# Performance work log

Measured on AMD Instinct MI355X. Metric: run time of the kernel, lower is better.

Reference implementation:

```python
import jax, jax.numpy as jnp
import numpy as np

B, N, OBS, H, HEADS = 8192, 32, 128, 256, 4
HD = H // HEADS  # head dim = 64
GAIN = (0.125 / H) ** 0.5
LN_EPS = 1e-5


def _ln(x):
    # LayerNorm over last dim, no affine (elementwise_affine=False)
    m = x.mean(axis=-1, keepdims=True)
    v = ((x - m) ** 2).mean(axis=-1, keepdims=True)
    return (x - m) * jax.lax.rsqrt(v + LN_EPS)


def setup_inputs() -> dict:
    key = jax.random.key(0)
    ks = jax.random.split(key, 20)
    f32 = jnp.float32
    # weights stored (in, out) so y = x @ W + b (transpose of torch layout)
    def w(k, i, o, g):
        return (jax.random.normal(k, (i, o), dtype=f32) * g)
    inp = {
        "all_agent_obs": jax.random.normal(ks[0], (B, N, OBS), dtype=f32),
        # EntityEmbedding (obs-only): 1-layer LinearEncoder, normal init * t-fixup gain
        "W_emb": w(ks[1], OBS, H, GAIN), "b_emb": jnp.zeros((H,), f32),
        # ResidualSelfAttention projections
        "Wq": w(ks[2], H, H, GAIN), "bq": jnp.zeros((H,), f32),
        "Wk": w(ks[3], H, H, GAIN), "bk": jnp.zeros((H,), f32),
        "Wv": w(ks[4], H, H, GAIN), "bv": jnp.zeros((H,), f32),
        "Wo": w(ks[5], H, H, GAIN), "bo": jnp.zeros((H,), f32),
        # LinearEncoder tail (num_layers=2), kaiming-ish scale * t-fixup gain
        "W1": w(ks[6], H, H, GAIN), "b1": jnp.zeros((H,), f32),
        "W2": w(ks[7], H, H, GAIN), "b2": jnp.zeros((H,), f32),
        # value head: Linear(h_size + 1, 1)
        "Wval": w(ks[8], H + 1, 1, (1.0 / (H + 1)) ** 0.5), "bval": jnp.zeros((1,), f32),
    }
    return inp


def reference(all_agent_obs, W_emb, b_emb, Wq, bq, Wk, bk, Wv, bv, Wo, bo,
              W1, b1, W2, b2, Wval, bval):
    # --- EntityEmbedding: 1-layer MLP with SiLU ---
    ent = jax.nn.silu(jnp.einsum("bno,oh->bnh", all_agent_obs, W_emb) + b_emb)

    # --- ResidualSelfAttention (pre-norm, no mask) ---
    x = _ln(ent)                                        # embedding_norm
    q = (x @ Wq + bq).reshape(B, N, HEADS, HD)
    k = (x @ Wk + bk).reshape(B, N, HEADS, HD)
    v = (x @ Wv + bv).reshape(B, N, HEADS, HD)
    attn = jnp.einsum("bnhd,bmhd->bhnm", q, k) / jnp.sqrt(jnp.float32(HD))
    attn = jax.nn.softmax(attn, axis=-1)
    out = jnp.einsum("bhnm,bmhd->bnhd", attn, v).reshape(B, N, H)
    out = _ln(out @ Wo + bo + x)                        # fc_out + residual, residual_norm
    pooled = out.mean(axis=1)                           # (B, H) unmasked avg pool

    # --- LinearEncoder tail (2 layers, SiLU) ---
    enc = jax.nn.silu(pooled @ W1 + b1)
    enc = jax.nn.silu(enc @ W2 + b2)

    # --- norm agent count: max_agents updates to N, so val = N*2/N - 1 = 1.0 ---
    nc = jnp.ones((B, 1), dtype=enc.dtype)
    enc = jnp.concatenate([enc, nc], axis=-1)           # (B, H+1)
    return enc @ Wval + bval                            # (B, 1)
```

## Files before the change

kernel.cpp:

```cpp
#include <hip/hip_runtime.h>


typedef __bf16 bf16x8 __attribute__((ext_vector_type(8)));
typedef float f32x4 __attribute__((ext_vector_type(4)));
typedef unsigned short ushort_t;

#define DEVI static __device__ __forceinline__
#define MFMA16(a, b, cc) __builtin_amdgcn_mfma_f32_16x16x32_bf16((a), (b), (cc), 0, 0, 0)

#define WAITV2 asm volatile("s_waitcnt vmcnt(2)" ::: "memory")
#define WAITV0 asm volatile("s_waitcnt vmcnt(0)" ::: "memory")
#define WAITLG asm volatile("s_waitcnt lgkmcnt(0)" ::: "memory")
#define BAR() __builtin_amdgcn_s_barrier()
#define SCHEDB() __builtin_amdgcn_sched_barrier(0)

constexpr int OWemb_ = 0;
constexpr int OWq_   = 32768;
constexpr int OWk_   = OWq_ + 65536;
constexpr int OWv_   = OWk_ + 65536;
constexpr int OWo_   = OWv_ + 65536;
constexpr int OW1_   = OWo_ + 65536;
constexpr int OW2_   = OW1_ + 65536;

constexpr int OBS_STRIDE = 264;
constexpr int L_BST = 32768;
constexpr int LDS_TOTAL = 32768 + 3 * 16384;
static_assert(LDS_TOTAL <= 81920, "need <=80KB for 2 blocks/CU");

DEVI float silu_f(float x) { return x / (1.0f + __expf(-x)); }
DEVI f32x4 splat4(float x) { f32x4 v = {x, x, x, x}; return v; }
DEVI uint2 pack4(f32x4 v) {
  union { __bf16 h[4]; uint2 u; } x;
  x.h[0] = (__bf16)v[0]; x.h[1] = (__bf16)v[1];
  x.h[2] = (__bf16)v[2]; x.h[3] = (__bf16)v[3];
  return x.u;
}
DEVI f32x4 unpk(uint2 u) {
  union { uint2 u2; __bf16 h[4]; } x; x.u2 = u;
  f32x4 v = {(float)x.h[0], (float)x.h[1], (float)x.h[2], (float)x.h[3]};
  return v;
}
DEVI bf16x8 ld_frag(const char* p) { return *(const bf16x8*)p; }
DEVI bf16x8 u4b(unsigned a, unsigned b, unsigned cc, unsigned d) {
  union { unsigned u[4]; bf16x8 v; } x;
  x.u[0] = a; x.u[1] = b; x.u[2] = cc; x.u[3] = d;
  return x.v;
}
DEVI unsigned to_agpr(unsigned v) {
  unsigned d;
  asm volatile("v_accvgpr_write_b32 %0, %1" : "=a"(d) : "v"(v));
  return d;
}
DEVI unsigned from_agpr(unsigned a) {
  unsigned d;
  asm volatile("v_accvgpr_read_b32 %0, %1" : "=v"(d) : "a"(a));
  return d;
}
DEVI int xaddr(int row, int k4) {
  int t = row >> 4, cc = row & 15;
  int ks = k4 >> 5, kg = (k4 >> 3) & 3, half = (k4 >> 2) & 1;
  return ((t * 8 + ks) * 64 + kg * 16 + cc) * 16 + half * 8;
}

typedef const __attribute__((address_space(1))) unsigned int* gas_ptr;
typedef __attribute__((address_space(3))) unsigned int* las_ptr;
DEVI void gload16(const void* g, void* l) {
  __builtin_amdgcn_global_load_lds((gas_ptr)g, (las_ptr)l, 16, 0, 0);
}

constexpr int CSRC(int p) {
  return (p < 4)  ? (OWemb_ + p * 8192)
       : (p < 12) ? (OWq_ + (p - 4) * 8192)
       : (p < 20) ? (OWk_ + (p - 12) * 8192)
       : (p < 28) ? (OWv_ + (p - 20) * 8192)
                  : (OWo_ + (p - 28) * 8192);
}

DEVI void issue_chunk(const ushort_t* pw, int srcOff, char* bst, int slot, int wv, int lane) {
  char* dst = bst + slot * 16384 + wv * 2048;
  const ushort_t* s = pw + srcOff + wv * 1024 + (size_t)lane * 8;
  gload16(s, dst);
  gload16(s + 512, dst + 1024);
}
#define PH_ISSUE(ch) issue_chunk(pw, CSRC(ch), bst, (ch) % 3, wv, lane)

__global__ void pack_weights(const float* __restrict__ Wemb, const float* __restrict__ Wq,
                             const float* __restrict__ Wk, const float* __restrict__ Wv,
                             const float* __restrict__ Wo, const float* __restrict__ W1,
                             const float* __restrict__ W2, ushort_t* __restrict__ ws) {
  int t = blockIdx.x * 256 + threadIdx.x;
  if (t >= 53248) return;
  const float* src;
  int dst, n, k0;
  if (t < 4096) {
    int rem = t & 1023;
    int ctg = rem >> 6, l = rem & 63;
    n = ctg * 16 + (l & 15);
    k0 = (t >> 10) * 32 + (l >> 4) * 8;
    src = Wemb; dst = OWemb_ + t * 8;
  } else if (t < 36864) {
    int u = t - 4096, m = u >> 13, loc = u & 8191;
    int rem = loc & 1023;
    int ctg = rem >> 6, l = rem & 63;
    n = ctg * 16 + (l & 15);
    k0 = (loc >> 10) * 32 + (l >> 4) * 8;
    src = (m == 0) ? Wq : (m == 1) ? Wk : (m == 2) ? Wv : Wo;
    dst = OWq_ + m * 65536 + loc * 8;
  } else {
    int u = t - 36864, m = u >> 13, loc = u & 8191;
    int ln = loc & 63, ks = (loc >> 6) & 7, ct = loc >> 9;
    n = ct * 16 + (ln & 15);
    k0 = ks * 32 + (ln >> 4) * 8;
    src = m ? W2 : W1; dst = OW1_ + m * 65536 + loc * 8;
  }
  union { __bf16 h[8]; uint4 u; } pk;
  #pragma unroll
  for (int j = 0; j < 8; ++j) pk.h[j] = (__bf16)src[(k0 + j) * 256 + n];
  *(uint4*)(ws + dst) = pk.u;
}

__global__ __launch_bounds__(512, 4)
void poca_fused(const float* __restrict__ obs, const ushort_t* __restrict__ pw,
                const float* __restrict__ b_emb, const float* __restrict__ bq,
                const float* __restrict__ bk, const float* __restrict__ bv,
                const float* __restrict__ bo, const float* __restrict__ b1,
                const float* __restrict__ b2, const float* __restrict__ Wval,
                const float* __restrict__ bval, float* __restrict__ out) {
  __shared__ __align__(128) char lds[LDS_TOTAL];
  const int tid = threadIdx.x;
  const int wv = tid >> 6, lane = tid & 63;
  const int g = lane >> 4, c = lane & 15;
  const int mg = wv >> 2, ng = wv & 3;
  char* xb = lds;
  char* bst = lds + L_BST;
  char* as_ = bst + wv * 4096;
  char* pp1 = bst;
  char* poolb = bst;
  char* y1b = bst + 8448;
  char* ptlb = bst + 16896;
  char* pp2 = bst + 20480;

  PH_ISSUE(0); PH_ISSUE(1);
  f32x4 bemb_r[4];
  #pragma unroll
  for (int ct = 0; ct < 4; ++ct) bemb_r[ct] = *(const f32x4*)(b_emb + ng * 64 + ct * 16 + g * 4);

  {
    const float4* op = (const float4*)(obs + (size_t)blockIdx.x * 64 * 128);
    #pragma unroll
    for (int it = 0; it < 4; ++it) {
      int idx = it * 512 + tid;
      float4 v = op[idx];
      int row = idx >> 5, col4 = idx & 31;
      union { __bf16 h[4]; uint2 u; } cv;
      cv.h[0] = (__bf16)v.x; cv.h[1] = (__bf16)v.y;
      cv.h[2] = (__bf16)v.z; cv.h[3] = (__bf16)v.w;
      *(uint2*)(xb + row * OBS_STRIDE + col4 * 8) = cv.u;
    }
  }
  WAITLG;

  f32x4 acc[2][4];

  #pragma unroll
  for (int p = 0; p < 4; ++p) {
    WAITV2; BAR();
    PH_ISSUE(p + 2);
    if (p == 0) {
      #pragma unroll
      for (int ct = 0; ct < 4; ++ct) { acc[0][ct] = bemb_r[ct]; acc[1][ct] = bemb_r[ct]; }
    }
    const char* ck = bst + (p % 3) * 16384;
    bf16x8 wf[4], xf[2];
    #pragma unroll
    for (int t = 0; t < 4; ++t) wf[t] = ld_frag(ck + ((ng * 4 + t) * 64 + lane) * 16);
    #pragma unroll
    for (int rt = 0; rt < 2; ++rt)
      xf[rt] = ld_frag(xb + ((mg * 2 + rt) * 16 + c) * OBS_STRIDE + p * 64 + g * 16);
    #pragma unroll
    for (int rt = 0; rt < 2; ++rt)
      #pragma unroll
      for (int ct = 0; ct < 4; ++ct) acc[rt][ct] = MFMA16(wf[ct], xf[rt], acc[rt][ct]);
    SCHEDB();
  }

  BAR();
  #pragma unroll
  for (int rt = 0; rt < 2; ++rt)
    #pragma unroll
    for (int ct = 0; ct < 4; ++ct)
      #pragma unroll
      for (int r = 0; r < 4; ++r) acc[rt][ct][r] = silu_f(acc[rt][ct][r]);
  #pragma unroll
  for (int rt = 0; rt < 2; ++rt) {
    float s1 = 0.f, s2 = 0.f;
    #pragma unroll
    for (int ct = 0; ct < 4; ++ct)
      #pragma unroll
      for (int r = 0; r < 4; ++r) { float e = acc[rt][ct][r]; s1 += e; s2 += e * e; }
    s1 += __shfl_xor(s1, 16); s2 += __shfl_xor(s2, 16);
    s1 += __shfl_xor(s1, 32); s2 += __shfl_xor(s2, 32);
    if (g == 0)
      *(float2*)(pp1 + (mg * 32 + rt * 16 + c) * 32 + ng * 8) = make_float2(s1, s2);
  }
  WAITLG; BAR();
  {
    float mu[2], rs[2];
    #pragma unroll
    for (int rt = 0; rt < 2; ++rt) {
      int row = mg * 32 + rt * 16 + c;
      f32x4 pA = *(const f32x4*)(pp1 + row * 32);
      f32x4 pB = *(const f32x4*)(pp1 + row * 32 + 16);
      float S1 = pA[0] + pA[2] + pB[0] + pB[2];
      float S2 = pA[1] + pA[3] + pB[1] + pB[3];
      float m_ = S1 * (1.f / 256.f);
      float v_ = S2 * (1.f / 256.f) - m_ * m_;
      mu[rt] = m_; rs[rt] = rsqrtf(v_ + 1e-5f);
    }
    #pragma unroll
    for (int rt = 0; rt < 2; ++rt)
      #pragma unroll
      for (int ct = 0; ct < 4; ++ct) {
        f32x4 xv;
        #pragma unroll
        for (int r = 0; r < 4; ++r) xv[r] = (acc[rt][ct][r] - mu[rt]) * rs[rt];
        *(uint2*)(xb + xaddr(mg * 32 + rt * 16 + c, ng * 64 + ct * 16 + g * 4)) = pack4(xv);
      }
  }
  f32x4 bq_r[4];
  #pragma unroll
  for (int ct = 0; ct < 4; ++ct) bq_r[ct] = *(const f32x4*)(bq + ng * 64 + ct * 16 + g * 4);
  SCHEDB();
  WAITLG; BAR();

  #pragma unroll
  for (int p = 4; p < 12; ++p) {
    WAITV2; BAR();
    PH_ISSUE(p + 2);
    if (p == 4) {
      #pragma unroll
      for (int ct = 0; ct < 4; ++ct) { acc[0][ct] = bq_r[ct]; acc[1][ct] = bq_r[ct]; }
    }
    const char* ck = bst + (p % 3) * 16384;
    const int ks = p - 4;
    bf16x8 wf[4], xf[2];
    #pragma unroll
    for (int t = 0; t < 4; ++t) wf[t] = ld_frag(ck + ((ng * 4 + t) * 64 + lane) * 16);
    #pragma unroll
    for (int rt = 0; rt < 2; ++rt)
      xf[rt] = ld_frag(xb + (((mg * 2 + rt) * 8 + ks) * 64 + lane) * 16);
    #pragma unroll
    for (int rt = 0; rt < 2; ++rt)
      #pragma unroll
      for (int ct = 0; ct < 4; ++ct) acc[rt][ct] = MFMA16(wf[ct], xf[rt], acc[rt][ct]);
    SCHEDB();
  }

  unsigned qs[16];
  #pragma unroll
  for (int rt = 0; rt < 2; ++rt)
    #pragma unroll
    for (int ct = 0; ct < 4; ++ct) {
      uint2 qp = pack4(acc[rt][ct]);
      qs[(rt * 4 + ct) * 2] = to_agpr(qp.x);
      qs[(rt * 4 + ct) * 2 + 1] = to_agpr(qp.y);
    }
  f32x4 bk_r[4];
  #pragma unroll
  for (int ct = 0; ct < 4; ++ct) bk_r[ct] = *(const f32x4*)(bk + ng * 64 + ct * 16 + g * 4);

  #pragma unroll
  for (int p = 12; p < 20; ++p) {
    if (p < 19) { WAITV2; } else { WAITV0; }
    BAR();
    if (p <= 17) PH_ISSUE(p + 2);
    if (p == 12) {
      #pragma unroll
      for (int ct = 0; ct < 4; ++ct) { acc[0][ct] = bk_r[ct]; acc[1][ct] = bk_r[ct]; }
    }
    const char* ck = bst + (p % 3) * 16384;
    const int ks = p - 12;
    bf16x8 wf[4], xf[2];
    #pragma unroll
    for (int t = 0; t < 4; ++t) wf[t] = ld_frag(ck + ((ng * 4 + t) * 64 + lane) * 16);
    #pragma unroll
    for (int rt = 0; rt < 2; ++rt)
      xf[rt] = ld_frag(xb + (((mg * 2 + rt) * 8 + ks) * 64 + lane) * 16);
    #pragma unroll
    for (int rt = 0; rt < 2; ++rt)
      #pragma unroll
      for (int ct = 0; ct < 4; ++ct) acc[rt][ct] = MFMA16(wf[ct], xf[rt], acc[rt][ct]);
    SCHEDB();
  }

  float rinv[2];
  uint2 p_pk[2][2];
  float bv_r[4];
  {
    BAR();
    f32x4 sacc[2][2];
    sacc[0][0] = splat4(0.f); sacc[0][1] = splat4(0.f);
    sacc[1][0] = splat4(0.f); sacc[1][1] = splat4(0.f);
    #pragma unroll
    for (int hf = 0; hf < 2; ++hf) {
      #pragma unroll
      for (int rt2 = 0; rt2 < 2; ++rt2)
        #pragma unroll
        for (int ctl = 0; ctl < 2; ++ctl) {
          int gr = ctl * 2 + (g >> 1);
          int off = rt2 * 1024 + (gr * 16 + c) * 16 + (g & 1) * 8;
          int qi = (rt2 * 4 + hf * 2 + ctl) * 2;
          *(uint2*)(as_ + off) = make_uint2(from_agpr(qs[qi]), from_agpr(qs[qi + 1]));
          *(uint2*)(as_ + 2048 + off) = pack4(acc[rt2][hf * 2 + ctl]);
        }
      WAITLG;
      bf16x8 qf[2], kf[2];
      #pragma unroll
      for (int t = 0; t < 2; ++t) {
        qf[t] = ld_frag(as_ + t * 1024 + lane * 16);
        kf[t] = ld_frag(as_ + 2048 + t * 1024 + lane * 16);
      }
      #pragma unroll
      for (int qt = 0; qt < 2; ++qt)
        #pragma unroll
        for (int kt = 0; kt < 2; ++kt)
          sacc[qt][kt] = MFMA16(kf[kt], qf[qt], sacc[qt][kt]);
    }
    #pragma unroll
    for (int qt = 0; qt < 2; ++qt) {
      float sc[2][4];
      float mx = -3e38f;
      #pragma unroll
      for (int kt = 0; kt < 2; ++kt)
        #pragma unroll
        for (int r = 0; r < 4; ++r) { sc[kt][r] = sacc[qt][kt][r] * 0.125f; mx = fmaxf(mx, sc[kt][r]); }
      mx = fmaxf(mx, __shfl_xor(mx, 16));
      mx = fmaxf(mx, __shfl_xor(mx, 32));
      float sm = 0.f;
      #pragma unroll
      for (int kt = 0; kt < 2; ++kt)
        #pragma unroll
        for (int r = 0; r < 4; ++r) { float e = __expf(sc[kt][r] - mx); sc[kt][r] = e; sm += e; }
      sm += __shfl_xor(sm, 16);
      sm += __shfl_xor(sm, 32);
      rinv[qt] = 1.0f / sm;
      #pragma unroll
      for (int kt = 0; kt < 2; ++kt) {
        f32x4 pv = {sc[kt][0], sc[kt][1], sc[kt][2], sc[kt][3]};
        p_pk[qt][kt] = pack4(pv);
      }
    }
    #pragma unroll
    for (int ct = 0; ct < 4; ++ct) bv_r[ct] = bv[ng * 64 + ct * 16 + c];
  }
  SCHEDB();
  WAITLG; BAR();
  PH_ISSUE(20); PH_ISSUE(21);

  #pragma unroll
  for (int p = 20; p < 28; ++p) {
    if (p < 27) { WAITV2; } else { WAITV0; }
    BAR();
    if (p <= 25) PH_ISSUE(p + 2);
    if (p == 20) {
      #pragma unroll
      for (int ct = 0; ct < 4; ++ct) {
        f32x4 b_ = splat4(bv_r[ct]);
        acc[0][ct] = b_; acc[1][ct] = b_;
      }
    }
    const char* ck = bst + (p % 3) * 16384;
    const int ks = p - 20;
    bf16x8 wf[4], xf[2];
    #pragma unroll
    for (int t = 0; t < 4; ++t) wf[t] = ld_frag(ck + ((ng * 4 + t) * 64 + lane) * 16);
    #pragma unroll
    for (int rt = 0; rt < 2; ++rt)
      xf[rt] = ld_frag(xb + (((mg * 2 + rt) * 8 + ks) * 64 + lane) * 16);
    #pragma unroll
    for (int rt = 0; rt < 2; ++rt)
      #pragma unroll
      for (int ct = 0; ct < 4; ++ct) acc[rt][ct] = MFMA16(xf[rt], wf[ct], acc[rt][ct]);
    SCHEDB();
  }

  {
    BAR();
    #pragma unroll
    for (int rt2 = 0; rt2 < 2; ++rt2)
      #pragma unroll
      for (int ct = 0; ct < 4; ++ct) {
        int gr = rt2 * 2 + (g >> 1);
        int off = ct * 1024 + (gr * 16 + c) * 16 + (g & 1) * 8;
        *(uint2*)(as_ + off) = pack4(acc[rt2][ct]);
      }
    uint2 respk[2][4];
    #pragma unroll
    for (int rt = 0; rt < 2; ++rt)
      #pragma unroll
      for (int ct = 0; ct < 4; ++ct)
        respk[rt][ct] = *(uint2*)(xb + xaddr(mg * 32 + rt * 16 + c, ng * 64 + ct * 16 + g * 4));
    f32x4 bo_r[4];
    #pragma unroll
    for (int ct = 0; ct < 4; ++ct) bo_r[ct] = *(const f32x4*)(bo + ng * 64 + ct * 16 + g * 4);
    WAITLG;
    bf16x8 vf[4];
    #pragma unroll
    for (int dt = 0; dt < 4; ++dt) vf[dt] = ld_frag(as_ + dt * 1024 + lane * 16);
    const int l1 = (g & 1) * 32 + c, l2 = l1 + 16;
    const bool hi = (g >= 2);
    #pragma unroll
    for (int qt = 0; qt < 2; ++qt) {
      unsigned x0k0 = __shfl(p_pk[qt][0].x, l1), x0k1 = __shfl(p_pk[qt][1].x, l1);
      unsigned y0k0 = __shfl(p_pk[qt][0].y, l1), y0k1 = __shfl(p_pk[qt][1].y, l1);
      unsigned x1k0 = __shfl(p_pk[qt][0].x, l2), x1k1 = __shfl(p_pk[qt][1].x, l2);
      unsigned y1k0 = __shfl(p_pk[qt][0].y, l2), y1k1 = __shfl(p_pk[qt][1].y, l2);
      bf16x8 pf = u4b(hi ? x0k1 : x0k0, hi ? y0k1 : y0k0, hi ? x1k1 : x1k0, hi ? y1k1 : y1k0);
      #pragma unroll
      for (int dt = 0; dt < 4; ++dt) {
        f32x4 o = splat4(0.f);
        o = MFMA16(vf[dt], pf, o);
        #pragma unroll
        for (int r = 0; r < 4; ++r) o[r] *= rinv[qt];
        *(uint2*)(xb + xaddr(mg * 32 + qt * 16 + c, ng * 64 + dt * 16 + g * 4)) = pack4(o);
      }
    }
    #pragma unroll
    for (int ct = 0; ct < 4; ++ct) {
      #pragma unroll
      for (int rt = 0; rt < 2; ++rt) acc[rt][ct] = bo_r[ct] + unpk(respk[rt][ct]);
    }
  }
  SCHEDB();
  WAITLG; BAR();
  PH_ISSUE(28); PH_ISSUE(29);

  #pragma unroll
  for (int p = 28; p < 36; ++p) {
    if (p < 35) { WAITV2; } else { WAITV0; }
    BAR();
    if (p <= 33) PH_ISSUE(p + 2);
    const char* ck = bst + (p % 3) * 16384;
    const int ks = p - 28;
    bf16x8 wf[4], xf[2];
    #pragma unroll
    for (int t = 0; t < 4; ++t) wf[t] = ld_frag(ck + ((ng * 4 + t) * 64 + lane) * 16);
    #pragma unroll
    for (int rt = 0; rt < 2; ++rt)
      xf[rt] = ld_frag(xb + (((mg * 2 + rt) * 8 + ks) * 64 + lane) * 16);
    #pragma unroll
    for (int rt = 0; rt < 2; ++rt)
      #pragma unroll
      for (int ct = 0; ct < 4; ++ct) acc[rt][ct] = MFMA16(wf[ct], xf[rt], acc[rt][ct]);
    SCHEDB();
  }

  BAR();
  #pragma unroll
  for (int rt = 0; rt < 2; ++rt) {
    float s1 = 0.f, s2 = 0.f;
    #pragma unroll
    for (int ct = 0; ct < 4; ++ct)
      #pragma unroll
      for (int r = 0; r < 4; ++r) { float e = acc[rt][ct][r]; s1 += e; s2 += e * e; }
    s1 += __shfl_xor(s1, 16); s2 += __shfl_xor(s2, 16);
    s1 += __shfl_xor(s1, 32); s2 += __shfl_xor(s2, 32);
    if (g == 0)
      *(float2*)(pp2 + (mg * 32 + rt * 16 + c) * 32 + ng * 8) = make_float2(s1, s2);
  }
  WAITLG; BAR();
  {
    float mu[2], rs[2];
    #pragma unroll
    for (int rt = 0; rt < 2; ++rt) {
      int row = mg * 32 + rt * 16 + c;
      f32x4 pA = *(const f32x4*)(pp2 + row * 32);
      f32x4 pB = *(const f32x4*)(pp2 + row * 32 + 16);
      float S1 = pA[0] + pA[2] + pB[0] + pB[2];
      float S2 = pA[1] + pA[3] + pB[1] + pB[3];
      float m_ = S1 * (1.f / 256.f);
      float v_ = S2 * (1.f / 256.f) - m_ * m_;
      mu[rt] = m_; rs[rt] = rsqrtf(v_ + 1e-5f);
    }
    f32x4 ps[4];
    #pragma unroll
    for (int ct = 0; ct < 4; ++ct) {
      #pragma unroll
      for (int r = 0; r < 4; ++r)
        ps[ct][r] = (acc[0][ct][r] - mu[0]) * rs[0] + (acc[1][ct][r] - mu[1]) * rs[1];
    }
    #pragma unroll
    for (int st = 1; st < 16; st <<= 1)
      #pragma unroll
      for (int ct = 0; ct < 4; ++ct)
        #pragma unroll
        for (int r = 0; r < 4; ++r) ps[ct][r] += __shfl_xor(ps[ct][r], st);
    if (c == 0) {
      #pragma unroll
      for (int ct = 0; ct < 4; ++ct) {
        f32x4 pv;
        #pragma unroll
        for (int r = 0; r < 4; ++r) pv[r] = ps[ct][r] * (1.f / 32.f);
        *(uint2*)(poolb + mg * 528 + (ng * 64 + ct * 16 + g * 4) * 2) = pack4(pv);
      }
    }
  }
  #pragma unroll
  for (int it = 0; it < 4; ++it) {
    int idx = it * 512 + tid;
    if (idx < 1792) {
      int row = 2 + (idx >> 7), col = idx & 127;
      *(unsigned*)(poolb + row * 528 + col * 4) = 0;
      *(unsigned*)(y1b + row * 528 + col * 4) = 0;
    }
  }
  WAITLG; BAR();

  f32x4 t1[2];
  #pragma unroll
  for (int ctl = 0; ctl < 2; ++ctl) t1[ctl] = splat4(b1[wv * 32 + ctl * 16 + c]);
  #pragma unroll
  for (int ks = 0; ks < 8; ++ks) {
    bf16x8 a = ld_frag(poolb + c * 528 + ks * 64 + g * 16);
    #pragma unroll
    for (int ctl = 0; ctl < 2; ++ctl) {
      bf16x8 b = *(const bf16x8*)(pw + OW1_ + (size_t)(((wv * 2 + ctl) * 8 + ks) * 64 + lane) * 8);
      t1[ctl] = MFMA16(a, b, t1[ctl]);
    }
  }
  if (g == 0) {
    #pragma unroll
    for (int ctl = 0; ctl < 2; ++ctl)
      #pragma unroll
      for (int r = 0; r < 4; ++r)
        *(__bf16*)(y1b + r * 528 + (wv * 32 + ctl * 16 + c) * 2) = (__bf16)silu_f(t1[ctl][r]);
  }
  WAITLG; BAR();
  f32x4 t2[2];
  #pragma unroll
  for (int ctl = 0; ctl < 2; ++ctl) t2[ctl] = splat4(b2[wv * 32 + ctl * 16 + c]);
  #pragma unroll
  for (int ks = 0; ks < 8; ++ks) {
    bf16x8 a = ld_frag(y1b + c * 528 + ks * 64 + g * 16);
    #pragma unroll
    for (int ctl = 0; ctl < 2; ++ctl) {
      bf16x8 b = *(const bf16x8*)(pw + OW2_ + (size_t)(((wv * 2 + ctl) * 8 + ks) * 64 + lane) * 8);
      t2[ctl] = MFMA16(a, b, t2[ctl]);
    }
  }
  if (g == 0) {
    float part[4] = {0.f, 0.f, 0.f, 0.f};
    #pragma unroll
    for (int ctl = 0; ctl < 2; ++ctl) {
      float wvv = Wval[wv * 32 + ctl * 16 + c];
      #pragma unroll
      for (int r = 0; r < 4; ++r) part[r] += silu_f(t2[ctl][r]) * wvv;
    }
    #pragma unroll
    for (int m = 1; m < 16; m <<= 1) {
      #pragma unroll
      for (int r = 0; r < 4; ++r) part[r] += __shfl_xor(part[r], m);
    }
    if (c == 0) {
      float4 p4 = make_float4(part[0], part[1], part[2], part[3]);
      *(float4*)(ptlb + wv * 16) = p4;
    }
  }
  WAITLG; BAR();
  if (tid < 2) {
    float s = Wval[256] + bval[0];
    const float* pt = (const float*)ptlb;
    #pragma unroll
    for (int w8 = 0; w8 < 8; ++w8) s += pt[w8 * 4 + tid];
    out[(size_t)blockIdx.x * 2 + tid] = s;
  }
}

extern "C" void kernel_launch(void* const* d_in, const int* in_sizes, int n_in,
                              void* d_out, int out_size, void* d_ws, size_t ws_size,
                              hipStream_t stream) {
  (void)in_sizes; (void)n_in; (void)out_size; (void)ws_size;
  const float* obs  = (const float*)d_in[0];
  const float* Wemb = (const float*)d_in[1];
  const float* bemb = (const float*)d_in[2];
  const float* Wq   = (const float*)d_in[3];
  const float* bq   = (const float*)d_in[4];
  const float* Wk   = (const float*)d_in[5];
  const float* bk   = (const float*)d_in[6];
  const float* Wv   = (const float*)d_in[7];
  const float* bv   = (const float*)d_in[8];
  const float* Wo   = (const float*)d_in[9];
  const float* bo   = (const float*)d_in[10];
  const float* W1   = (const float*)d_in[11];
  const float* b1   = (const float*)d_in[12];
  const float* W2   = (const float*)d_in[13];
  const float* b2   = (const float*)d_in[14];
  const float* Wval = (const float*)d_in[15];
  const float* bval = (const float*)d_in[16];
  ushort_t* ws = (ushort_t*)d_ws;
  float* out = (float*)d_out;

  pack_weights<<<208, 256, 0, stream>>>(Wemb, Wq, Wk, Wv, Wo, W1, W2, ws);
  poca_fused<<<4096, 512, 0, stream>>>(obs, ws, bemb, bq, bk, bv, bo, b1, b2, Wval, bval, out);
}
```

Measured before the change: 320.1 us.

## Prefetch weight chunks earlier, fold V bias into PV MFMA, add MFMA priority

```diff
diff --git a/kernel.cpp b/kernel.cpp
--- a/kernel.cpp
+++ b/kernel.cpp
@@ -13,6 +13,8 @@
 #define WAITLG asm volatile("s_waitcnt lgkmcnt(0)" ::: "memory")
 #define BAR() __builtin_amdgcn_s_barrier()
 #define SCHEDB() __builtin_amdgcn_sched_barrier(0)
+#define PRIO1() __builtin_amdgcn_s_setprio(1)
+#define PRIO0() __builtin_amdgcn_s_setprio(0)
 
 constexpr int OWemb_ = 0;
 constexpr int OWq_   = 32768;
@@ -134,6 +136,7 @@
   char* xb = lds;
   char* bst = lds + L_BST;
   char* as_ = bst + wv * 4096;
+  char* as2 = (wv < 4) ? (bst + wv * 4096) : (bst + 32768 + (wv - 4) * 4096);
   char* pp1 = bst;
   char* poolb = bst;
   char* y1b = bst + 8448;
@@ -177,10 +180,12 @@
     #pragma unroll
     for (int rt = 0; rt < 2; ++rt)
       xf[rt] = ld_frag(xb + ((mg * 2 + rt) * 16 + c) * OBS_STRIDE + p * 64 + g * 16);
+    PRIO1();
     #pragma unroll
     for (int rt = 0; rt < 2; ++rt)
       #pragma unroll
       for (int ct = 0; ct < 4; ++ct) acc[rt][ct] = MFMA16(wf[ct], xf[rt], acc[rt][ct]);
+    PRIO0();
     SCHEDB();
   }
 
@@ -249,10 +254,12 @@
     #pragma unroll
     for (int rt = 0; rt < 2; ++rt)
       xf[rt] = ld_frag(xb + (((mg * 2 + rt) * 8 + ks) * 64 + lane) * 16);
+    PRIO1();
     #pragma unroll
     for (int rt = 0; rt < 2; ++rt)
       #pragma unroll
       for (int ct = 0; ct < 4; ++ct) acc[rt][ct] = MFMA16(wf[ct], xf[rt], acc[rt][ct]);
+    PRIO0();
     SCHEDB();
   }
 
@@ -286,18 +293,19 @@
     #pragma unroll
     for (int rt = 0; rt < 2; ++rt)
       xf[rt] = ld_frag(xb + (((mg * 2 + rt) * 8 + ks) * 64 + lane) * 16);
+    PRIO1();
     #pragma unroll
     for (int rt = 0; rt < 2; ++rt)
       #pragma unroll
       for (int ct = 0; ct < 4; ++ct) acc[rt][ct] = MFMA16(wf[ct], xf[rt], acc[rt][ct]);
+    PRIO0();
     SCHEDB();
   }
 
-  float rinv[2];
   uint2 p_pk[2][2];
-  float bv_r[4];
   {
     BAR();
+    PH_ISSUE(20);
     f32x4 sacc[2][2];
     sacc[0][0] = splat4(0.f); sacc[0][1] = splat4(0.f);
     sacc[1][0] = splat4(0.f); sacc[1][1] = splat4(0.f);
@@ -343,19 +351,17 @@
         for (int r = 0; r < 4; ++r) { float e = __expf(sc[kt][r] - mx); sc[kt][r] = e; sm += e; }
       sm += __shfl_xor(sm, 16);
       sm += __shfl_xor(sm, 32);
-      rinv[qt] = 1.0f / sm;
+      float ri = 1.0f / sm;
       #pragma unroll
       for (int kt = 0; kt < 2; ++kt) {
-        f32x4 pv = {sc[kt][0], sc[kt][1], sc[kt][2], sc[kt][3]};
+        f32x4 pv = {sc[kt][0] * ri, sc[kt][1] * ri, sc[kt][2] * ri, sc[kt][3] * ri};
         p_pk[qt][kt] = pack4(pv);
       }
     }
-    #pragma unroll
-    for (int ct = 0; ct < 4; ++ct) bv_r[ct] = bv[ng * 64 + ct * 16 + c];
   }
   SCHEDB();
   WAITLG; BAR();
-  PH_ISSUE(20); PH_ISSUE(21);
+  PH_ISSUE(21);
 
   #pragma unroll
   for (int p = 20; p < 28; ++p) {
@@ -364,10 +370,7 @@
     if (p <= 25) PH_ISSUE(p + 2);
     if (p == 20) {
       #pragma unroll
-      for (int ct = 0; ct < 4; ++ct) {
-        f32x4 b_ = splat4(bv_r[ct]);
-        acc[0][ct] = b_; acc[1][ct] = b_;
-      }
+      for (int ct = 0; ct < 4; ++ct) { acc[0][ct] = splat4(0.f); acc[1][ct] = splat4(0.f); }
     }
     const char* ck = bst + (p % 3) * 16384;
     const int ks = p - 20;
@@ -377,22 +380,25 @@
     #pragma unroll
     for (int rt = 0; rt < 2; ++rt)
       xf[rt] = ld_frag(xb + (((mg * 2 + rt) * 8 + ks) * 64 + lane) * 16);
+    PRIO1();
     #pragma unroll
     for (int rt = 0; rt < 2; ++rt)
       #pragma unroll
       for (int ct = 0; ct < 4; ++ct) acc[rt][ct] = MFMA16(xf[rt], wf[ct], acc[rt][ct]);
+    PRIO0();
     SCHEDB();
   }
 
   {
     BAR();
+    PH_ISSUE(28);
     #pragma unroll
     for (int rt2 = 0; rt2 < 2; ++rt2)
       #pragma unroll
       for (int ct = 0; ct < 4; ++ct) {
         int gr = rt2 * 2 + (g >> 1);
         int off = ct * 1024 + (gr * 16 + c) * 16 + (g & 1) * 8;
-        *(uint2*)(as_ + off) = pack4(acc[rt2][ct]);
+        *(uint2*)(as2 + off) = pack4(acc[rt2][ct]);
       }
     uint2 respk[2][4];
     #pragma unroll
@@ -400,13 +406,16 @@
       #pragma unroll
       for (int ct = 0; ct < 4; ++ct)
         respk[rt][ct] = *(uint2*)(xb + xaddr(mg * 32 + rt * 16 + c, ng * 64 + ct * 16 + g * 4));
-    f32x4 bo_r[4];
-    #pragma unroll
-    for (int ct = 0; ct < 4; ++ct) bo_r[ct] = *(const f32x4*)(bo + ng * 64 + ct * 16 + g * 4);
+    f32x4 bo_r[4], bvp[4];
+    #pragma unroll
+    for (int ct = 0; ct < 4; ++ct) {
+      bo_r[ct] = *(const f32x4*)(bo + ng * 64 + ct * 16 + g * 4);
+      bvp[ct]  = *(const f32x4*)(bv + ng * 64 + ct * 16 + g * 4);
+    }
     WAITLG;
     bf16x8 vf[4];
     #pragma unroll
-    for (int dt = 0; dt < 4; ++dt) vf[dt] = ld_frag(as_ + dt * 1024 + lane * 16);
+    for (int dt = 0; dt < 4; ++dt) vf[dt] = ld_frag(as2 + dt * 1024 + lane * 16);
     const int l1 = (g & 1) * 32 + c, l2 = l1 + 16;
     const bool hi = (g >= 2);
     #pragma unroll
@@ -418,10 +427,7 @@
       bf16x8 pf = u4b(hi ? x0k1 : x0k0, hi ? y0k1 : y0k0, hi ? x1k1 : x1k0, hi ? y1k1 : y1k0);
       #pragma unroll
       for (int dt = 0; dt < 4; ++dt) {
-        f32x4 o = splat4(0.f);
-        o = MFMA16(vf[dt], pf, o);
-        #pragma unroll
-        for (int r = 0; r < 4; ++r) o[r] *= rinv[qt];
+        f32x4 o = MFMA16(vf[dt], pf, bvp[dt]);
         *(uint2*)(xb + xaddr(mg * 32 + qt * 16 + c, ng * 64 + dt * 16 + g * 4)) = pack4(o);
       }
     }
@@ -433,7 +439,7 @@
   }
   SCHEDB();
   WAITLG; BAR();
-  PH_ISSUE(28); PH_ISSUE(29);
+  PH_ISSUE(29);
 
   #pragma unroll
   for (int p = 28; p < 36; ++p) {
@@ -448,10 +454,12 @@
     #pragma unroll
     for (int rt = 0; rt < 2; ++rt)
       xf[rt] = ld_frag(xb + (((mg * 2 + rt) * 8 + ks) * 64 + lane) * 16);
+    PRIO1();
     #pragma unroll
     for (int rt = 0; rt < 2; ++rt)
       #pragma unroll
       for (int ct = 0; ct < 4; ++ct) acc[rt][ct] = MFMA16(wf[ct], xf[rt], acc[rt][ct]);
+    PRIO0();
     SCHEDB();
   }
 
```

After: 329.8 us. +3.0%, slower.
